# Kernel tuning notes

Measured on AMD Instinct MI355X. Metric: run time of the kernel, lower is better.

Reference implementation:

```python
import jax, jax.numpy as jnp
import numpy as np

D = 64      # voxel grid resolution
N = 65536   # active voxels
C = 512     # channels
H = 2048    # mlp hidden = 4*C
EPS = 1e-6


def setup_inputs() -> dict:
    key = jax.random.key(0)
    ks = jax.random.split(key, 8)
    # unique sparse voxel coords (submanifold conv assumes no duplicates)
    rng = np.random.default_rng(0)
    lin = rng.choice(D * D * D, size=N, replace=False)
    coords = jnp.asarray(np.stack([lin // (D * D), (lin // D) % D, lin % D], axis=1), dtype=jnp.int32)  # [N,3]
    s = 1.0 / np.sqrt(C)
    return {
        'feats': jax.random.normal(ks[0], (N, C), jnp.float32),
        'coords': coords,
        'conv_w': jax.random.normal(ks[1], (3, 3, 3, C, C), jnp.float32) * (s / np.sqrt(27.0)),
        'conv_b': jax.random.normal(ks[2], (C,), jnp.float32) * 0.02,
        'ln_g': jnp.ones((C,), jnp.float32),
        'ln_b': jnp.zeros((C,), jnp.float32),
        'w1': jax.random.normal(ks[3], (C, H), jnp.float32) * s,
        'b1': jnp.zeros((H,), jnp.float32),
        'w2': jax.random.normal(ks[4], (H, C), jnp.float32) * (1.0 / np.sqrt(H)),
        'b2': jnp.zeros((C,), jnp.float32),
    }


def _sparse_conv3x3x3(feats, coords, conv_w, conv_b):
    # submanifold sparse conv: out[i] = b + sum_{offsets} feats[nbr(i,off)] @ W[off]
    n = feats.shape[0]
    # padded dense index grid: grid[x+1,y+1,z+1] = voxel row index, -1 = empty
    grid = jnp.full((D + 2, D + 2, D + 2), -1, dtype=jnp.int32)
    grid = grid.at[coords[:, 0] + 1, coords[:, 1] + 1, coords[:, 2] + 1].set(
        jnp.arange(n, dtype=jnp.int32))
    h = jnp.broadcast_to(conv_b, feats.shape).astype(feats.dtype)
    for dx in (0, 1, 2):
        for dy in (0, 1, 2):
            for dz in (0, 1, 2):
                nbr = grid[coords[:, 0] + dx, coords[:, 1] + dy, coords[:, 2] + dz]  # [N]
                valid = (nbr >= 0)
                g = feats[jnp.where(valid, nbr, 0)] * valid[:, None].astype(feats.dtype)  # [N,C]
                h = h + g @ conv_w[dx, dy, dz]
    return h


def reference(feats, coords, conv_w, conv_b, ln_g, ln_b, w1, b1, w2, b2):
    h = _sparse_conv3x3x3(feats, coords, conv_w, conv_b)          # [N,C]
    # LayerNorm32: normalize in fp32, eps=1e-6, affine
    h32 = h.astype(jnp.float32)
    mu = jnp.mean(h32, axis=-1, keepdims=True)
    var = jnp.mean(jnp.square(h32 - mu), axis=-1, keepdims=True)
    nf = ((h32 - mu) * jax.lax.rsqrt(var + EPS) * ln_g + ln_b).astype(feats.dtype)
    # SiLU MLP + residual
    out = jax.nn.silu(nf @ w1 + b1) @ w2 + b2 + feats
    return out
```

## Files before the change

kernel.cpp:

```cpp
#include <hip/hip_runtime.h>

typedef __attribute__((ext_vector_type(8))) short short8;
typedef __attribute__((ext_vector_type(4))) float f32x4;
typedef __attribute__((ext_vector_type(4))) float f4v;
typedef unsigned short u16;
typedef unsigned int u32;

#define NPTS 65536
#define CCH 512
#define GDIM 66
#define GDIM2 (66*66)
#define CAPO 18432
#define TPO1 144

__device__ __forceinline__ u16 f2bf(float f) {
    u32 u = __builtin_bit_cast(u32, f);
    u32 r = (u + 0x7fffu + ((u >> 16) & 1u)) >> 16;
    return (u16)r;
}
__device__ __forceinline__ u16 f2bt(float f) {
    return (u16)(__builtin_bit_cast(u32, f) >> 16);
}
__device__ __forceinline__ float bf2f(u16 h) {
    u32 u = ((u32)h) << 16;
    return __builtin_bit_cast(float, u);
}
__device__ __forceinline__ float fexp2(float x) { return __builtin_amdgcn_exp2f(x); }
__device__ __forceinline__ float frcp(float x)  { return __builtin_amdgcn_rcpf(x); }

__device__ __forceinline__ void gld16(const void* g, void* l) {
    __builtin_amdgcn_global_load_lds((const __attribute__((address_space(1))) void*)g,
                                     (__attribute__((address_space(3))) void*)l, 16, 0, 0);
}


__global__ void scatter_vox(const int* __restrict__ coords, int* __restrict__ grid) {
    int i = blockIdx.x * 256 + threadIdx.x;
    if (i < NPTS) {
        int c0 = coords[3*i], c1 = coords[3*i+1], c2 = coords[3*i+2];
        grid[(c0+1)*GDIM2 + (c1+1)*GDIM + (c2+1)] = i;
    }
}

__global__ void cast_bf16(const float* __restrict__ in, u16* __restrict__ out, int n8) {
    int i = blockIdx.x * 256 + threadIdx.x;
    if (i >= n8) return;
    f4v a = *(const f4v*)(in + (size_t)i*8);
    f4v b = *(const f4v*)(in + (size_t)i*8 + 4);
    short8 o;
    #pragma unroll
    for (int j = 0; j < 4; ++j) { o[j] = (short)f2bf(a[j]); o[j+4] = (short)f2bf(b[j]); }
    *(short8*)(out + (size_t)i*8) = o;
}

__global__ void transpose_cast(const float* __restrict__ in, u16* __restrict__ out,
                               int R, int Cc) {
    __shared__ float tile[32][33];
    size_t moff = (size_t)blockIdx.z * R * Cc;
    in += moff; out += moff;
    int tx = threadIdx.x, ty = threadIdx.y;
    #pragma unroll
    for (int j = 0; j < 4; ++j) {
        int r = blockIdx.y*32 + ty + j*8;
        int c = blockIdx.x*32 + tx;
        tile[ty + j*8][tx] = in[(size_t)r*Cc + c];
    }
    __syncthreads();
    #pragma unroll
    for (int j = 0; j < 4; ++j) {
        int orow = blockIdx.x*32 + ty + j*8;
        int ocol = blockIdx.y*32 + tx;
        out[(size_t)orow*R + ocol] = f2bf(tile[tx][ty + j*8]);
    }
}


__device__ __forceinline__ int nbr_lookup(const int* coords, const int* grid, int i, int o) {
    int dx = o / 9, dy = (o / 3) % 3, dz = o % 3;
    int c0 = coords[3*i], c1 = coords[3*i+1], c2 = coords[3*i+2];
    return grid[(c0+dx)*GDIM2 + (c1+dy)*GDIM + (c2+dz)];
}

__global__ __launch_bounds__(256) void count_valid(const int* __restrict__ coords,
        const int* __restrict__ grid, int* __restrict__ blockCnt) {
    int o1 = blockIdx.y;
    int o = o1 + (o1 >= 13);
    int i = blockIdx.x*256 + threadIdx.x;
    int v = nbr_lookup(coords, grid, i, o);
    unsigned long long b = __ballot(v >= 0);
    __shared__ int wc[4];
    if ((threadIdx.x & 63) == 0) wc[threadIdx.x >> 6] = __popcll(b);
    __syncthreads();
    if (threadIdx.x == 0)
        blockCnt[o1*256 + blockIdx.x] = wc[0]+wc[1]+wc[2]+wc[3];
}

__global__ __launch_bounds__(256) void scan_kernel(const int* __restrict__ blockCnt,
        int* __restrict__ blockOff, int* __restrict__ cnt) {
    int o1 = blockIdx.x;
    int t = threadIdx.x, lane = t & 63, w = t >> 6;
    __shared__ int wsum[4];
    int v = blockCnt[o1*256 + t];
    int x = v;
    #pragma unroll
    for (int s = 1; s < 64; s <<= 1) {
        int y = __shfl_up(x, s);
        if (lane >= s) x += y;
    }
    if (lane == 63) wsum[w] = x;
    __syncthreads();
    int base = 0;
    for (int k = 0; k < w; ++k) base += wsum[k];
    blockOff[o1*256 + t] = base + x - v;
    if (t == 255) cnt[o1] = base + x;
}

__global__ __launch_bounds__(256) void fill_kernel(const int* __restrict__ coords,
        const int* __restrict__ grid, const int* __restrict__ blockOff,
        int* __restrict__ srcIdx, int* __restrict__ posMap) {
    int o1 = blockIdx.y;
    int o = o1 + (o1 >= 13);
    int i = blockIdx.x*256 + threadIdx.x;
    int v = nbr_lookup(coords, grid, i, o);
    bool valid = v >= 0;
    unsigned long long b = __ballot(valid);
    int lane = threadIdx.x & 63, w = threadIdx.x >> 6;
    __shared__ int wc[4];
    if (lane == 0) wc[w] = __popcll(b);
    __syncthreads();
    int base = blockOff[o1*256 + blockIdx.x];
    for (int k = 0; k < w; ++k) base += wc[k];
    int pre = __popcll(b & ((1ull << lane) - 1ull));
    int pos = base + pre;
    bool ok = valid && pos < CAPO;
    if (ok) srcIdx[o1*CAPO + pos] = v;
    posMap[(size_t)o1*NPTS + i] = ok ? pos : -1;
}


template<int MODE, int NX, int RES, int LDOUT>
__global__ __launch_bounds__(256, 4) void gemm128(
    const u16* __restrict__ A, int lda,
    const u16* __restrict__ BT, int ldb,
    int nT,
    const float* __restrict__ bias,
    const u16* __restrict__ fbres,
    const float* __restrict__ fres,
    float* __restrict__ outf, u16* __restrict__ outb)
{
    __shared__ __align__(1024) char ldsA[16384];
    __shared__ __align__(1024) char ldsB[16384];
    const int L = blockIdx.x;
    const int cx = L & 7, tt0 = L >> 3;
    const int bx = tt0 % NX;
    const int by = cx + 8 * (tt0 / NX);
    const int row0 = by * 128, col0 = bx * 128;

    const int t = threadIdx.x;
    const int w = t >> 6, lane = t & 63;
    const int wm = w >> 1, wn = w & 1;
    const int ccsrc = (lane & 7) ^ (lane >> 3);
    const int laneRow = lane >> 3;

    f32x4 acc[4][4] = {};

    const u16* aptr[4];
    const u16* bptr[4];
    #pragma unroll
    for (int it = 0; it < 4; ++it) {
        int r = w*32 + it*8 + laneRow;
        aptr[it] = A + (size_t)(row0 + r)*lda + ccsrc*8;
        bptr[it] = BT + (size_t)(col0 + r)*ldb + ccsrc*8;
    }

    #pragma unroll 1
    for (int ks = 0; ks < nT; ++ks) {
        int k0 = ks * 64;
        #pragma unroll
        for (int it = 0; it < 4; ++it) {
            int c = w*256 + it*64 + lane;
            gld16(aptr[it] + k0, ldsA + c*16);
            gld16(bptr[it] + k0, ldsB + c*16);
        }
        __syncthreads();
        #pragma unroll
        for (int kk = 0; kk < 2; ++kk) {
            short8 a[4], b[4];
            #pragma unroll
            for (int f = 0; f < 4; ++f) {
                int rowA = wm*64 + f*16 + (lane & 15);
                int ch = (kk*4 + (lane >> 4)) ^ (lane & 7);
                a[f] = *(const short8*)(void*)(ldsA + rowA*128 + ch*16);
                int rowB = wn*64 + f*16 + (lane & 15);
                b[f] = *(const short8*)(void*)(ldsB + rowB*128 + ch*16);
            }
            #pragma unroll
            for (int i = 0; i < 4; ++i)
                #pragma unroll
                for (int j = 0; j < 4; ++j)
                    acc[i][j] = __builtin_amdgcn_mfma_f32_16x16x32_bf16(a[i], b[j], acc[i][j], 0, 0, 0);
        }
        __syncthreads();
    }

    #pragma unroll
    for (int i = 0; i < 4; ++i) {
        int r = row0 + wm*64 + i*16 + (lane >> 4)*4;
        #pragma unroll
        for (int j = 0; j < 4; ++j) {
            int c = col0 + wn*64 + j*16 + (lane & 15);
            float bv = bias[c];
            #pragma unroll
            for (int q = 0; q < 4; ++q) {
                float v = acc[i][j][q];
                if constexpr (MODE == 1) {
                    float val = v + bv;
                    float sg = frcp(1.f + fexp2(val * -1.44269504f));
                    outb[(size_t)(r+q)*LDOUT + c] = f2bt(val * sg);
                } else if constexpr (MODE == 2) {
                    size_t ix = (size_t)(r+q)*LDOUT + c;
                    float rsd = RES ? bf2f(fbres[ix]) : fres[ix];
                    outf[ix] = v + bv + rsd;
                } else {
                    outb[(size_t)(r+q)*LDOUT + c] = f2bt(v + bv);
                }
            }
        }
    }
}

__global__ __launch_bounds__(256, 4) void comp_gemm(
    const u16* __restrict__ fb,
    const int* __restrict__ srcIdx,
    const int* __restrict__ cnt,
    const u16* __restrict__ wcT,
    u16* __restrict__ comp,
    int o1base)
{
    __shared__ __align__(1024) char ldsA[16384];
    __shared__ __align__(1024) char ldsB[16384];
    const int L = blockIdx.x;
    const int cx = L & 7, tt0 = L >> 3;
    const int bx = tt0 & 3;
    const int y  = cx + 8 * (tt0 >> 2);
    const int o1loc = y / TPO1, mt = y % TPO1;
    const int o1 = o1base + o1loc;
    const int n = cnt[o1];
    if (mt * 128 >= n) return;
    const int o = o1 + (o1 >= 13);
    const int t = threadIdx.x;
    const int w = t >> 6, lane = t & 63;
    const int wm = w >> 1, wn = w & 1;
    const int col0 = bx * 128;
    const int ccsrc = (lane & 7) ^ (lane >> 3);
    const int laneRow = lane >> 3;

    const int* sIdx = srcIdx + o1*CAPO + mt*128;
    const u16* wb = wcT + ((size_t)o << 18);

    const u16* aptr[4];
    const u16* bptr[4];
    #pragma unroll
    for (int it = 0; it < 4; ++it) {
        int rloc = w*32 + it*8 + laneRow;
        int src = (mt*128 + rloc < n) ? sIdx[rloc] : NPTS;
        aptr[it] = fb + (size_t)src*512 + ccsrc*8;
        bptr[it] = wb + (size_t)(col0 + rloc)*512 + ccsrc*8;
    }

    f32x4 acc[4][4] = {};

    #pragma unroll 1
    for (int ks = 0; ks < 8; ++ks) {
        int k0 = ks * 64;
        #pragma unroll
        for (int it = 0; it < 4; ++it) {
            int c = w*256 + it*64 + lane;
            gld16(aptr[it] + k0, ldsA + c*16);
            gld16(bptr[it] + k0, ldsB + c*16);
        }
        __syncthreads();
        #pragma unroll
        for (int kk = 0; kk < 2; ++kk) {
            short8 a[4], b[4];
            #pragma unroll
            for (int f = 0; f < 4; ++f) {
                int rowA = wm*64 + f*16 + (lane & 15);
                int ch = (kk*4 + (lane >> 4)) ^ (lane & 7);
                a[f] = *(const short8*)(void*)(ldsA + rowA*128 + ch*16);
                int rowB = wn*64 + f*16 + (lane & 15);
                b[f] = *(const short8*)(void*)(ldsB + rowB*128 + ch*16);
            }
            #pragma unroll
            for (int i = 0; i < 4; ++i)
                #pragma unroll
                for (int j = 0; j < 4; ++j)
                    acc[i][j] = __builtin_amdgcn_mfma_f32_16x16x32_bf16(a[i], b[j], acc[i][j], 0, 0, 0);
        }
        __syncthreads();
    }

    #pragma unroll
    for (int i = 0; i < 4; ++i) {
        #pragma unroll
        for (int q = 0; q < 4; ++q) {
            int rl = wm*64 + i*16 + (lane >> 4)*4 + q;
            if (mt*128 + rl < n) {
                u16* cr = comp + ((size_t)(o1loc*CAPO + mt*128 + rl))*512
                               + col0 + wn*64 + (lane & 15);
                #pragma unroll
                for (int j = 0; j < 4; ++j)
                    cr[j*16] = f2bt(acc[i][j][q]);
            }
        }
    }
}


template<int FINAL>
__global__ __launch_bounds__(512) void reduce_kernel(
    const u16* __restrict__ comp, const int* __restrict__ posMap,
    int o1base, int nOff,
    u16* __restrict__ hc,
    const float* __restrict__ g, const float* __restrict__ bb,
    u16* __restrict__ nf)
{
    int w = threadIdx.x >> 6, lane = threadIdx.x & 63;
    int i = blockIdx.x*8 + w;
    u16* hr = hc + (size_t)i*512 + lane*8;
    short8 hv = *(const short8*)hr;
    float x[8];
    #pragma unroll
    for (int j = 0; j < 8; ++j) x[j] = bf2f((u16)hv[j]);

    #pragma unroll 1
    for (int k = 0; k < nOff; ++k) {
        int pos = posMap[(size_t)(o1base + k)*NPTS + i];
        if (pos >= 0) {
            short8 cv = *(const short8*)(comp + ((size_t)k*CAPO + pos)*512 + lane*8);
            #pragma unroll
            for (int j = 0; j < 8; ++j) x[j] += bf2f((u16)cv[j]);
        }
    }

    if constexpr (!FINAL) {
        short8 o;
        #pragma unroll
        for (int j = 0; j < 8; ++j) o[j] = (short)f2bf(x[j]);
        *(short8*)hr = o;
    } else {
        float s = 0.f, ss = 0.f;
        #pragma unroll
        for (int j = 0; j < 8; ++j) { s += x[j]; ss += x[j]*x[j]; }
        #pragma unroll
        for (int m = 1; m < 64; m <<= 1) { s += __shfl_xor(s, m); ss += __shfl_xor(ss, m); }
        float mu = s * (1.f/512.f);
        float var = ss * (1.f/512.f) - mu*mu;
        float inv = rsqrtf(var + 1e-6f);
        short8 o;
        #pragma unroll
        for (int j = 0; j < 8; ++j) {
            int c = lane*8 + j;
            o[j] = (short)f2bf((x[j] - mu) * inv * g[c] + bb[c]);
        }
        *(short8*)(nf + (size_t)i*512 + lane*8) = o;
    }
}


extern "C" void kernel_launch(void* const* d_in, const int* in_sizes, int n_in,
                              void* d_out, int out_size, void* d_ws, size_t ws_size,
                              hipStream_t stream) {
    const float* feats  = (const float*)d_in[0];
    const int*   coords = (const int*)d_in[1];
    const float* conv_w = (const float*)d_in[2];
    const float* conv_b = (const float*)d_in[3];
    const float* ln_g   = (const float*)d_in[4];
    const float* ln_b   = (const float*)d_in[5];
    const float* w1     = (const float*)d_in[6];
    const float* b1     = (const float*)d_in[7];
    const float* w2     = (const float*)d_in[8];
    const float* b2     = (const float*)d_in[9];
    float* out = (float*)d_out;
    char* ws = (char*)d_ws;

    size_t off = 0;
    auto take = [&](size_t bytes) -> void* {
        void* p = ws + off;
        off += (bytes + 1023) & ~(size_t)1023;
        return p;
    };
    int* grid_i   = (int*)take((size_t)GDIM*GDIM2*4);
    u16* wcT      = (u16*)take(27ull*512*512*2);
    u16* w1T      = (u16*)take(2048ull*512*2);
    u16* w2T      = (u16*)take(512ull*2048*2);
    u16* fb       = (u16*)take((NPTS+1ull)*512*2);
    int* srcIdx   = (int*)take(26ull*CAPO*4);
    int* posMap   = (int*)take(26ull*NPTS*4);
    int* blockCnt = (int*)take(26*256*4);
    int* blockOff = (int*)take(26*256*4);
    int* cnt      = (int*)take(26*4);

    const size_t nf_b     = 67108864ull;
    const size_t comp13_b = 13ull*CAPO*512*2;
    const size_t hc_b     = 67108864ull;
    const size_t slack    = 65536;

    bool sepNF = (off + nf_b + comp13_b + hc_b + slack) <= ws_size;

    u16* nf   = sepNF ? (u16*)take(nf_b) : fb;
    u16* comp = (u16*)take(comp13_b);
    u16* hc   = (u16*)take(hc_b);
    u16* g1   = comp;

    hipMemsetAsync(grid_i, 0xFF, (size_t)GDIM*GDIM2*4, stream);
    hipMemsetAsync(fb + (size_t)NPTS*512, 0, 512*2, stream);

    scatter_vox<<<NPTS/256, 256, 0, stream>>>(coords, grid_i);
    cast_bf16<<<(NPTS*CCH/8)/256, 256, 0, stream>>>(feats, fb, NPTS*CCH/8);
    transpose_cast<<<dim3(16,16,27), dim3(32,8), 0, stream>>>(conv_w, wcT, 512, 512);
    transpose_cast<<<dim3(64,16,1),  dim3(32,8), 0, stream>>>(w1, w1T, 512, 2048);
    transpose_cast<<<dim3(16,64,1),  dim3(32,8), 0, stream>>>(w2, w2T, 2048, 512);

    count_valid<<<dim3(256,26), 256, 0, stream>>>(coords, grid_i, blockCnt);
    scan_kernel<<<26, 256, 0, stream>>>(blockCnt, blockOff, cnt);
    fill_kernel<<<dim3(256,26), 256, 0, stream>>>(coords, grid_i, blockOff, srcIdx, posMap);

    gemm128<3,4,0,512><<<2048, 256, 0, stream>>>(
        fb, 512, wcT + (13ull << 18), 512, 8, conv_b,
        nullptr, nullptr, nullptr, hc);

    comp_gemm<<<4*TPO1*13, 256, 0, stream>>>(fb, srcIdx, cnt, wcT, comp, 0);
    reduce_kernel<0><<<NPTS/8, 512, 0, stream>>>(comp, posMap, 0, 13, hc, nullptr, nullptr, nullptr);
    comp_gemm<<<4*TPO1*13, 256, 0, stream>>>(fb, srcIdx, cnt, wcT, comp, 13);
    reduce_kernel<1><<<NPTS/8, 512, 0, stream>>>(comp, posMap, 13, 13, hc, ln_g, ln_b, nf);

    gemm128<1,16,0,2048><<<8192, 256, 0, stream>>>(
        nf, 512, w1T, 512, 8, b1, nullptr, nullptr, nullptr, g1);

    if (sepNF) {
        gemm128<2,4,1,512><<<2048, 256, 0, stream>>>(
            g1, 2048, w2T, 2048, 32, b2, fb, nullptr, out, nullptr);
    } else {
        gemm128<2,4,0,512><<<2048, 256, 0, stream>>>(
            g1, 2048, w2T, 2048, 32, b2, nullptr, feats, out, nullptr);
    }
}
```

Measured before the change: 959.2 us.

## Triple-buffer GEMM K-loop with async LDS prefetch two tiles ahead

Both the dense GEMM and the gathered conv GEMM replace the load-sync-compute-sync loop with a 3-stage LDS ring over 32-wide K tiles. Global loads are issued two tiles ahead and waited on with explicit vmcnt, leaving one barrier per step. MFMA sections run at raised wave priority. In exchange, LDS per block rises to 48KB and launch bounds drop to 3 blocks per CU, and the smaller K step doubles the number of barriers.

```diff
diff --git a/kernel.cpp b/kernel.cpp
--- a/kernel.cpp
+++ b/kernel.cpp
@@ -32,6 +32,37 @@
     __builtin_amdgcn_global_load_lds((const __attribute__((address_space(1))) void*)g,
                                      (__attribute__((address_space(3))) void*)l, 16, 0, 0);
 }
+
+#define PIPE_LOOP(NT32)                                                                \
+    stageT(0, 0); stageT(1, 1);                                                        \
+    {                                                                                  \
+        int cur = 0, sb = 2;                                                           \
+        _Pragma("unroll 1")                                                            \
+        for (int t = 0; t < (NT32); ++t) {                                             \
+            __builtin_amdgcn_sched_barrier(0);                                         \
+            if (t + 1 < (NT32)) asm volatile("s_waitcnt vmcnt(4)" ::: "memory");       \
+            else                asm volatile("s_waitcnt vmcnt(0)" ::: "memory");       \
+            __builtin_amdgcn_s_barrier();                                              \
+            __builtin_amdgcn_sched_barrier(0);                                         \
+            if (t + 2 < (NT32)) { stageT(sb, t + 2); sb = (sb == 2) ? 0 : sb + 1; }    \
+            const char* la = lds + cur * 16384;                                        \
+            const char* lb = la + 8192;                                                \
+            cur = (cur == 2) ? 0 : cur + 1;                                            \
+            short8 a[4], b[4];                                                         \
+            _Pragma("unroll")                                                          \
+            for (int f = 0; f < 4; ++f) {                                              \
+                a[f] = *(const short8*)(const void*)(la + (wm*64 + f*16 + rbase)*64 + chx*16); \
+                b[f] = *(const short8*)(const void*)(lb + (wn*64 + f*16 + rbase)*64 + chx*16); \
+            }                                                                          \
+            __builtin_amdgcn_s_setprio(1);                                             \
+            _Pragma("unroll")                                                          \
+            for (int i = 0; i < 4; ++i)                                                \
+                _Pragma("unroll")                                                      \
+                for (int j = 0; j < 4; ++j)                                            \
+                    acc[i][j] = __builtin_amdgcn_mfma_f32_16x16x32_bf16(a[i], b[j], acc[i][j], 0, 0, 0); \
+            __builtin_amdgcn_s_setprio(0);                                             \
+        }                                                                              \
+    }
 
 
 __global__ void scatter_vox(const int* __restrict__ coords, int* __restrict__ grid) {
@@ -139,69 +170,47 @@
 
 
 template<int MODE, int NX, int RES, int LDOUT>
-__global__ __launch_bounds__(256, 4) void gemm128(
+__global__ __launch_bounds__(256, 3) void gemm128(
     const u16* __restrict__ A, int lda,
     const u16* __restrict__ BT, int ldb,
-    int nT,
+    int nT32,
     const float* __restrict__ bias,
     const u16* __restrict__ fbres,
     const float* __restrict__ fres,
     float* __restrict__ outf, u16* __restrict__ outb)
 {
-    __shared__ __align__(1024) char ldsA[16384];
-    __shared__ __align__(1024) char ldsB[16384];
+    __shared__ __align__(1024) char lds[49152];
     const int L = blockIdx.x;
     const int cx = L & 7, tt0 = L >> 3;
     const int bx = tt0 % NX;
     const int by = cx + 8 * (tt0 / NX);
     const int row0 = by * 128, col0 = bx * 128;
 
-    const int t = threadIdx.x;
-    const int w = t >> 6, lane = t & 63;
+    const int tid = threadIdx.x;
+    const int w = tid >> 6, lane = tid & 63;
     const int wm = w >> 1, wn = w & 1;
-    const int ccsrc = (lane & 7) ^ (lane >> 3);
-    const int laneRow = lane >> 3;
+    const int rI = tid >> 2;
+    const int csrc = (tid & 3) ^ ((tid >> 3) & 3);
+    const int rbase = lane & 15;
+    const int chx = (lane >> 4) ^ ((lane >> 1) & 3);
 
     f32x4 acc[4][4] = {};
 
-    const u16* aptr[4];
-    const u16* bptr[4];
-    #pragma unroll
-    for (int it = 0; it < 4; ++it) {
-        int r = w*32 + it*8 + laneRow;
-        aptr[it] = A + (size_t)(row0 + r)*lda + ccsrc*8;
-        bptr[it] = BT + (size_t)(col0 + r)*ldb + ccsrc*8;
-    }
-
-    #pragma unroll 1
-    for (int ks = 0; ks < nT; ++ks) {
-        int k0 = ks * 64;
-        #pragma unroll
-        for (int it = 0; it < 4; ++it) {
-            int c = w*256 + it*64 + lane;
-            gld16(aptr[it] + k0, ldsA + c*16);
-            gld16(bptr[it] + k0, ldsB + c*16);
-        }
-        __syncthreads();
-        #pragma unroll
-        for (int kk = 0; kk < 2; ++kk) {
-            short8 a[4], b[4];
-            #pragma unroll
-            for (int f = 0; f < 4; ++f) {
-                int rowA = wm*64 + f*16 + (lane & 15);
-                int ch = (kk*4 + (lane >> 4)) ^ (lane & 7);
-                a[f] = *(const short8*)(void*)(ldsA + rowA*128 + ch*16);
-                int rowB = wn*64 + f*16 + (lane & 15);
-                b[f] = *(const short8*)(void*)(ldsB + rowB*128 + ch*16);
-            }
-            #pragma unroll
-            for (int i = 0; i < 4; ++i)
-                #pragma unroll
-                for (int j = 0; j < 4; ++j)
-                    acc[i][j] = __builtin_amdgcn_mfma_f32_16x16x32_bf16(a[i], b[j], acc[i][j], 0, 0, 0);
-        }
-        __syncthreads();
-    }
+    const u16* aP0 = A + (size_t)(row0 + rI) * lda + csrc*8;
+    const u16* aP1 = aP0 + (size_t)64 * lda;
+    const u16* bP0 = BT + (size_t)(col0 + rI) * ldb + csrc*8;
+    const u16* bP1 = bP0 + (size_t)64 * ldb;
+
+    auto stageT = [&](int buf, int tt) {
+        char* la = lds + buf*16384;
+        int k0 = tt * 32;
+        gld16(aP0 + k0, la + tid*16);
+        gld16(aP1 + k0, la + 4096 + tid*16);
+        gld16(bP0 + k0, la + 8192 + tid*16);
+        gld16(bP1 + k0, la + 12288 + tid*16);
+    };
+
+    PIPE_LOOP(nT32)
 
     #pragma unroll
     for (int i = 0; i < 4; ++i) {
@@ -229,7 +238,7 @@
     }
 }
 
-__global__ __launch_bounds__(256, 4) void comp_gemm(
+__global__ __launch_bounds__(256, 3) void comp_gemm(
     const u16* __restrict__ fb,
     const int* __restrict__ srcIdx,
     const int* __restrict__ cnt,
@@ -237,8 +246,7 @@
     u16* __restrict__ comp,
     int o1base)
 {
-    __shared__ __align__(1024) char ldsA[16384];
-    __shared__ __align__(1024) char ldsB[16384];
+    __shared__ __align__(1024) char lds[49152];
     const int L = blockIdx.x;
     const int cx = L & 7, tt0 = L >> 3;
     const int bx = tt0 & 3;
@@ -248,57 +256,37 @@
     const int n = cnt[o1];
     if (mt * 128 >= n) return;
     const int o = o1 + (o1 >= 13);
-    const int t = threadIdx.x;
-    const int w = t >> 6, lane = t & 63;
+    const int tid = threadIdx.x;
+    const int w = tid >> 6, lane = tid & 63;
     const int wm = w >> 1, wn = w & 1;
     const int col0 = bx * 128;
-    const int ccsrc = (lane & 7) ^ (lane >> 3);
-    const int laneRow = lane >> 3;
+    const int rI = tid >> 2;
+    const int csrc = (tid & 3) ^ ((tid >> 3) & 3);
+    const int rbase = lane & 15;
+    const int chx = (lane >> 4) ^ ((lane >> 1) & 3);
 
     const int* sIdx = srcIdx + o1*CAPO + mt*128;
     const u16* wb = wcT + ((size_t)o << 18);
 
-    const u16* aptr[4];
-    const u16* bptr[4];
-    #pragma unroll
-    for (int it = 0; it < 4; ++it) {
-        int rloc = w*32 + it*8 + laneRow;
-        int src = (mt*128 + rloc < n) ? sIdx[rloc] : NPTS;
-        aptr[it] = fb + (size_t)src*512 + ccsrc*8;
-        bptr[it] = wb + (size_t)(col0 + rloc)*512 + ccsrc*8;
-    }
+    int src0 = (mt*128 + rI      < n) ? sIdx[rI]      : NPTS;
+    int src1 = (mt*128 + 64 + rI < n) ? sIdx[64 + rI] : NPTS;
+    const u16* aP0 = fb + (size_t)src0*512 + csrc*8;
+    const u16* aP1 = fb + (size_t)src1*512 + csrc*8;
+    const u16* bP0 = wb + (size_t)(col0 + rI)*512 + csrc*8;
+    const u16* bP1 = bP0 + (size_t)64*512;
 
     f32x4 acc[4][4] = {};
 
-    #pragma unroll 1
-    for (int ks = 0; ks < 8; ++ks) {
-        int k0 = ks * 64;
-        #pragma unroll
-        for (int it = 0; it < 4; ++it) {
-            int c = w*256 + it*64 + lane;
-            gld16(aptr[it] + k0, ldsA + c*16);
-            gld16(bptr[it] + k0, ldsB + c*16);
-        }
-        __syncthreads();
-        #pragma unroll
-        for (int kk = 0; kk < 2; ++kk) {
-            short8 a[4], b[4];
-            #pragma unroll
-            for (int f = 0; f < 4; ++f) {
-                int rowA = wm*64 + f*16 + (lane & 15);
-                int ch = (kk*4 + (lane >> 4)) ^ (lane & 7);
-                a[f] = *(const short8*)(void*)(ldsA + rowA*128 + ch*16);
-                int rowB = wn*64 + f*16 + (lane & 15);
-                b[f] = *(const short8*)(void*)(ldsB + rowB*128 + ch*16);
-            }
-            #pragma unroll
-            for (int i = 0; i < 4; ++i)
-                #pragma unroll
-                for (int j = 0; j < 4; ++j)
-                    acc[i][j] = __builtin_amdgcn_mfma_f32_16x16x32_bf16(a[i], b[j], acc[i][j], 0, 0, 0);
-        }
-        __syncthreads();
-    }
+    auto stageT = [&](int buf, int tt) {
+        char* la = lds + buf*16384;
+        int k0 = tt * 32;
+        gld16(aP0 + k0, la + tid*16);
+        gld16(aP1 + k0, la + 4096 + tid*16);
+        gld16(bP0 + k0, la + 8192 + tid*16);
+        gld16(bP1 + k0, la + 12288 + tid*16);
+    };
+
+    PIPE_LOOP(16)
 
     #pragma unroll
     for (int i = 0; i < 4; ++i) {
@@ -427,7 +415,7 @@
     fill_kernel<<<dim3(256,26), 256, 0, stream>>>(coords, grid_i, blockOff, srcIdx, posMap);
 
     gemm128<3,4,0,512><<<2048, 256, 0, stream>>>(
-        fb, 512, wcT + (13ull << 18), 512, 8, conv_b,
+        fb, 512, wcT + (13ull << 18), 512, 16, conv_b,
         nullptr, nullptr, nullptr, hc);
 
     comp_gemm<<<4*TPO1*13, 256, 0, stream>>>(fb, srcIdx, cnt, wcT, comp, 0);
@@ -436,13 +424,13 @@
     reduce_kernel<1><<<NPTS/8, 512, 0, stream>>>(comp, posMap, 13, 13, hc, ln_g, ln_b, nf);
 
     gemm128<1,16,0,2048><<<8192, 256, 0, stream>>>(
-        nf, 512, w1T, 512, 8, b1, nullptr, nullptr, nullptr, g1);
+        nf, 512, w1T, 512, 16, b1, nullptr, nullptr, nullptr, g1);
 
     if (sepNF) {
         gemm128<2,4,1,512><<<2048, 256, 0, stream>>>(
-            g1, 2048, w2T, 2048, 32, b2, fb, nullptr, out, nullptr);
+            g1, 2048, w2T, 2048, 64, b2, fb, nullptr, out, nullptr);
     } else {
         gemm128<2,4,0,512><<<2048, 256, 0, stream>>>(
-            g1, 2048, w2T, 2048, 32, b2, nullptr, feats, out, nullptr);
-    }
-}
+            g1, 2048, w2T, 2048, 64, b2, nullptr, feats, out, nullptr);
+    }
+}
```

After: 1.038 ms. 8.2% more time.
